# Kernel tuning notes

Measured on AMD Instinct MI355X. Metric: run time of the kernel, lower is better.

## Reference

```python
import jax, jax.numpy as jnp
import numpy as np

# CRF hyperparameters (match torch module defaults / init_kwargs)
W_BILATERAL = 1.0
W_GAUSSIAN = 1.0
SIG_B_SPATIAL = 5.0
SIG_B_COLOR = 0.5
SIG_G_SPATIAL = 5.0
UPDATE_FACTOR = 3.0
KERNEL_RANGE = 1
ITERATIONS = 5


def _coords(H, W, dtype):
    gy, gx = jnp.meshgrid(jnp.arange(H, dtype=dtype), jnp.arange(W, dtype=dtype), indexing='ij')
    return jnp.stack([gy, gx])  # [2, H, W]


def _gauss_kernel(feat):
    # feat: [B, N, D] -> dense Gaussian affinity [B, N, N] = exp(-0.5 ||f_i - f_j||^2)
    sq = jnp.sum(feat * feat, axis=-1)  # [B, N]
    d2 = sq[:, :, None] + sq[:, None, :] - 2.0 * jnp.einsum('bnd,bmd->bnm', feat, feat)
    return jnp.exp(-0.5 * jnp.maximum(d2, 0.0))


def setup_inputs() -> dict:
    key = jax.random.key(0)
    k1, k2 = jax.random.split(key)
    return {
        'input_tensor': jax.random.normal(k1, (1, 5, 96, 96), dtype=jnp.float32),
        'reference_tensor': jax.random.uniform(k2, (1, 3, 96, 96), dtype=jnp.float32),
    }


def reference(input_tensor, reference_tensor):
    B, C, H, W = input_tensor.shape
    N = H * W
    coords = jnp.broadcast_to(_coords(H, W, reference_tensor.dtype)[None], (B, 2, H, W))
    # bilateral features: scaled coords ++ scaled color -> [B, N, 2+Cref]
    bfeat = jnp.concatenate([coords / SIG_B_SPATIAL, reference_tensor / SIG_B_COLOR], axis=1)
    bfeat = bfeat.reshape(B, -1, N).transpose(0, 2, 1)
    gfeat = (coords / SIG_G_SPATIAL).reshape(B, 2, N).transpose(0, 2, 1)
    # features are fixed across iterations -> precompute dense filter kernels once
    Kb = _gauss_kernel(bfeat)  # [B, N, N]
    Kg = _gauss_kernel(gfeat)  # [B, N, N]
    ksz = 2 * KERNEL_RANGE + 1
    # Potts model compatibility kernel: (1 - I) constant over the 3x3 window
    comp = jnp.broadcast_to((1.0 - jnp.eye(C, dtype=input_tensor.dtype))[:, :, None, None], (C, C, ksz, ksz))
    out = jax.nn.softmax(input_tensor, axis=1)
    for _ in range(ITERATIONS):
        flat = out.reshape(B, C, N)
        comb = (W_BILATERAL * jnp.einsum('bnm,bcm->bcn', Kb, flat)
                + W_GAUSSIAN * jnp.einsum('bnm,bcm->bcn', Kg, flat)).reshape(B, C, H, W)
        comb = jnp.pad(comb, ((0, 0), (0, 0), (KERNEL_RANGE, KERNEL_RANGE), (KERNEL_RANGE, KERNEL_RANGE)), mode='edge')
        upd = jax.lax.conv_general_dilated(comb, comp, (1, 1), 'VALID',
                                           dimension_numbers=('NCHW', 'OIHW', 'NCHW'))
        out = jax.nn.softmax(input_tensor - UPDATE_FACTOR * upd, axis=1)
    return out
```

## Files before the change

kernel.cpp:

```cpp
#include <hip/hip_runtime.h>
#include <math.h>

#define HH 96
#define WW 96
#define NN (HH*WW)
#define RAD 30

__device__ __forceinline__ float np_expf(float x) {
    float q = __builtin_rintf(x * 1.442695040888963f);
    float r = fmaf(q, -6.93145752e-1f, x);
    r = fmaf(q, -1.42860677e-6f, r);
    float num = 5.082762527590693718096e-04f;
    num = fmaf(num, r, 6.757896990527504603057e-03f);
    num = fmaf(num, r, 5.114512081637298353406e-02f);
    num = fmaf(num, r, 2.473615434895520810817e-01f);
    num = fmaf(num, r, 7.257664613233124478488e-01f);
    num = fmaf(num, r, 9.999999999980870924916e-01f);
    float den = 2.159509375685829852307e-02f;
    den = fmaf(den, r, -2.742335390411667452936e-01f);
    den = fmaf(den, r, 1.0f);
    float p = num / den;
    p = ldexpf(p, (int)q);
    if (x > 88.72283935546875f) p = __builtin_inff();
    if (x < -103.97208404541015625f) p = 0.0f;
    return p;
}

__device__ __forceinline__ float np_expf_nc(float x) {
    float q = __builtin_rintf(x * 1.442695040888963f);
    float r = fmaf(q, -6.93145752e-1f, x);
    r = fmaf(q, -1.42860677e-6f, r);
    float num = 5.082762527590693718096e-04f;
    num = fmaf(num, r, 6.757896990527504603057e-03f);
    num = fmaf(num, r, 5.114512081637298353406e-02f);
    num = fmaf(num, r, 2.473615434895520810817e-01f);
    num = fmaf(num, r, 7.257664613233124478488e-01f);
    num = fmaf(num, r, 9.999999999980870924916e-01f);
    float den = 2.159509375685829852307e-02f;
    den = fmaf(den, r, -2.742335390411667452936e-01f);
    den = fmaf(den, r, 1.0f);
    float p = num / den;
    return ldexpf(p, (int)q);
}

__global__ __launch_bounds__(256) void crf_prep(const float* __restrict__ input,
                                                const float* __restrict__ ref,
                                                float4* __restrict__ colA,
                                                float4* __restrict__ qA,
                                                float* __restrict__ qB) {
#pragma clang fp contract(off)
    int n = blockIdx.x * 256 + threadIdx.x;
    if (n >= NN) return;
    int py = n / WW;
    int px = n - py * WW;
    float yb = (float)py / 5.0f;
    float xb = (float)px / 5.0f;
    float r2 = ref[0 * NN + n] * 2.0f;
    float g2 = ref[1 * NN + n] * 2.0f;
    float b2 = ref[2 * NN + n] * 2.0f;
    float sqg = yb * yb + xb * xb;
    float sqb = ((sqg + r2 * r2) + g2 * g2) + b2 * b2;
    colA[n] = make_float4(r2, g2, b2, sqb);
    float l0 = input[0 * NN + n], l1 = input[1 * NN + n], l2 = input[2 * NN + n];
    float l3 = input[3 * NN + n], l4 = input[4 * NN + n];
    float m = fmaxf(fmaxf(fmaxf(fmaxf(l0, l1), l2), l3), l4);
    float e0 = np_expf(l0 - m), e1 = np_expf(l1 - m), e2 = np_expf(l2 - m);
    float e3 = np_expf(l3 - m), e4 = np_expf(l4 - m);
    float s = (((e0 + e1) + e2) + e3) + e4;
    qA[n] = make_float4(e0 / s, e1 / s, e2 / s, e3 / s);
    qB[n] = e4 / s;
}

__global__ __launch_bounds__(256) void crf_filter(const float4* __restrict__ colA,
                                                  const float4* __restrict__ qA,
                                                  const float* __restrict__ qB,
                                                  float* __restrict__ combF) {
#pragma clang fp contract(off)
    __shared__ float c5[HH];
    __shared__ float sq1[HH];
    __shared__ float cg[8][5];
    int tid = threadIdx.x;
    if (tid < HH) {
        float v = (float)tid / 5.0f;
        c5[tid] = v;
        sq1[tid] = v * v;
    }
    __syncthreads();

    int br = blockIdx.x / 12;
    int bc = blockIdx.x - br * 12;
    int row = (br & 1) ? (48 + (br >> 1)) : (47 - (br >> 1));
    int cg8 = (bc & 1) ? (6 + (bc >> 1)) : (5 - (bc >> 1));

    int j = tid & 3;
    int k = (tid >> 2) & 3;
    int p = (tid >> 4) & 7;
    int role = tid >> 7;
    int n0 = row * WW + cg8 * 8 + p;
    int py = row;
    int px = cg8 * 8 + p;
    float yn = c5[py], xn = c5[px];
    float sqg_n = sq1[py] + sq1[px];
    float4 cn = colA[n0];
    float sqb_n = cn.w;
    int ylo = py - RAD; if (ylo < 0) ylo = 0;
    int yhi = py + RAD; if (yhi > HH - 1) yhi = HH - 1;
    int xlo = px - RAD; if (xlo < 0) xlo = 0;
    int xhi = px + RAD; if (xhi > WW - 1) xhi = WW - 1;
    int res = k * 4 + j;
    int cst = xlo + ((res - xlo) & 15);

    float a0 = 0.f, a1 = 0.f, a2 = 0.f, a3 = 0.f, a4 = 0.f;
    if (role == 0) {
#pragma unroll 2
        for (int my = ylo; my <= yhi; ++my) {
            float ym = c5[my];
            float tyy = yn * ym;
            int rb = my * WW;
            for (int mx = cst; mx <= xhi; mx += 16) {
                int m = rb + mx;
                float4 cm = colA[m];
                float4 f = qA[m];
                float fb = qB[m];
                float dot = tyy;
                dot = dot + xn * c5[mx];
                dot = dot + cn.x * cm.x;
                dot = dot + cn.y * cm.y;
                dot = dot + cn.z * cm.z;
                float d2 = (sqb_n + cm.w) - 2.0f * dot;
                d2 = fmaxf(d2, 0.0f);
                float w = np_expf_nc(-0.5f * d2);
                a0 = a0 + w * f.x;
                a1 = a1 + w * f.y;
                a2 = a2 + w * f.z;
                a3 = a3 + w * f.w;
                a4 = a4 + w * fb;
            }
        }
    } else {
#pragma unroll 2
        for (int my = ylo; my <= yhi; ++my) {
            float ym = c5[my];
            float tyy = yn * ym;
            float sqy = sq1[my];
            int rb = my * WW;
            for (int mx = cst; mx <= xhi; mx += 16) {
                int m = rb + mx;
                float4 f = qA[m];
                float fb = qB[m];
                float dot = tyy;
                dot = dot + xn * c5[mx];
                float sqm = sqy + sq1[mx];
                float d2 = (sqg_n + sqm) - 2.0f * dot;
                d2 = fmaxf(d2, 0.0f);
                float w = np_expf_nc(-0.5f * d2);
                a0 = a0 + w * f.x;
                a1 = a1 + w * f.y;
                a2 = a2 + w * f.z;
                a3 = a3 + w * f.w;
                a4 = a4 + w * fb;
            }
        }
    }
    float r_[5] = {a0, a1, a2, a3, a4};
#pragma unroll
    for (int c = 0; c < 5; ++c) {
        float v = r_[c];
        v = v + __shfl_xor(v, 4);
        v = v + __shfl_xor(v, 8);
        v = v + __shfl_xor(v, 2);
        v = v + __shfl_xor(v, 1);
        r_[c] = v;
    }
    if (role == 1 && (tid & 15) == 0) {
#pragma unroll
        for (int c = 0; c < 5; ++c) cg[p][c] = r_[c];
    }
    __syncthreads();
    if (role == 0 && (tid & 15) == 0) {
#pragma unroll
        for (int c = 0; c < 5; ++c) combF[c * NN + n0] = r_[c] + cg[p][c];
    }
}

__global__ __launch_bounds__(256) void crf_update(const float* __restrict__ input,
                                                  const float* __restrict__ combF,
                                                  float4* __restrict__ qA,
                                                  float* __restrict__ qB,
                                                  float* __restrict__ outp,
                                                  int writeOut) {
#pragma clang fp contract(off)
    int n = blockIdx.x * 256 + threadIdx.x;
    if (n >= NN) return;
    int py = n / WW;
    int px = n - py * WW;
    float v[3][3][5];
#pragma unroll
    for (int ky = 0; ky < 3; ++ky) {
        int yy = py + ky - 1; yy = yy < 0 ? 0 : (yy > HH - 1 ? HH - 1 : yy);
#pragma unroll
        for (int kx = 0; kx < 3; ++kx) {
            int xx = px + kx - 1; xx = xx < 0 ? 0 : (xx > WW - 1 ? WW - 1 : xx);
            int m = yy * WW + xx;
#pragma unroll
            for (int c = 0; c < 5; ++c) v[ky][kx][c] = combF[c * NN + m];
        }
    }
    float l[5];
#pragma unroll
    for (int o = 0; o < 5; ++o) {
        float u = 0.f;
#pragma unroll
        for (int ky = 0; ky < 3; ++ky) {
#pragma unroll
            for (int kx = 0; kx < 3; ++kx) {
                float t = 0.f;
#pragma unroll
                for (int ci = 0; ci < 5; ++ci)
                    if (ci != o) t = t + v[ky][kx][ci];
                u = u + t;
            }
        }
        l[o] = input[o * NN + n] - 3.0f * u;
    }
    float m = fmaxf(fmaxf(fmaxf(fmaxf(l[0], l[1]), l[2]), l[3]), l[4]);
    float e0 = np_expf(l[0] - m), e1 = np_expf(l[1] - m), e2 = np_expf(l[2] - m);
    float e3 = np_expf(l[3] - m), e4 = np_expf(l[4] - m);
    float s = (((e0 + e1) + e2) + e3) + e4;
    float o0 = e0 / s, o1 = e1 / s, o2 = e2 / s, o3 = e3 / s, o4 = e4 / s;
    qA[n] = make_float4(o0, o1, o2, o3);
    qB[n] = o4;
    if (writeOut) {
        outp[0 * NN + n] = o0;
        outp[1 * NN + n] = o1;
        outp[2 * NN + n] = o2;
        outp[3 * NN + n] = o3;
        outp[4 * NN + n] = o4;
    }
}

extern "C" void kernel_launch(void* const* d_in, const int* in_sizes, int n_in,
                              void* d_out, int out_size, void* d_ws, size_t ws_size,
                              hipStream_t stream) {
    const float* input = (const float*)d_in[0];
    const float* ref = (const float*)d_in[1];
    float* ws = (float*)d_ws;
    float4* colA = (float4*)(ws + 0 * NN);
    float4* qA = (float4*)(ws + 4 * NN);
    float* qB = ws + 8 * NN;
    float* combF = ws + 9 * NN;
    float* outp = (float*)d_out;

    crf_prep<<<36, 256, 0, stream>>>(input, ref, colA, qA, qB);
    for (int it = 0; it < 5; ++it) {
        crf_filter<<<1152, 256, 0, stream>>>(colA, qA, qB, combF);
        crf_update<<<36, 256, 0, stream>>>(input, combF, qA, qB, outp, it == 4 ? 1 : 0);
    }
}
```

Baseline: 423.3 us.

## Cache truncated filter weights on first iteration and reuse in later iterations

After: 455.1 us. 1.08x slower.

```diff
diff --git a/kernel.cpp b/kernel.cpp
--- a/kernel.cpp
+++ b/kernel.cpp
@@ -5,6 +5,7 @@
 #define WW 96
 #define NN (HH*WW)
 #define RAD 30
+#define TOTPAIRS 24265476
 
 __device__ __forceinline__ float np_expf(float x) {
     float q = __builtin_rintf(x * 1.442695040888963f);
@@ -41,6 +42,17 @@
     den = fmaf(den, r, 1.0f);
     float p = num / den;
     return ldexpf(p, (int)q);
+}
+
+__device__ __forceinline__ int wincnt(int x) {
+    int lo = x - RAD; if (lo < 0) lo = 0;
+    int hi = x + RAD; if (hi > 95) hi = 95;
+    return hi - lo + 1;
+}
+__device__ __forceinline__ int cumwin(int x) {
+    int g1 = (x <= 30) ? (30 * x - (x * (x - 1)) / 2) : 465;
+    int g2 = (x <= 66) ? 0 : ((x - 66) * (x - 65)) / 2;
+    return 61 * x - g1 - g2;
 }
 
 __global__ __launch_bounds__(256) void crf_prep(const float* __restrict__ input,
@@ -71,6 +83,183 @@
     qB[n] = e4 / s;
 }
 
+#define FILTER_PREAMBLE                                                        \
+    int tid = threadIdx.x;                                                     \
+    int br = blockIdx.x / 12;                                                  \
+    int bc = blockIdx.x - br * 12;                                             \
+    int row = (br & 1) ? (48 + (br >> 1)) : (47 - (br >> 1));                  \
+    int cg8 = (bc & 1) ? (6 + (bc >> 1)) : (5 - (bc >> 1));                    \
+    int j = tid & 3;                                                           \
+    int k = (tid >> 2) & 3;                                                    \
+    int p = (tid >> 4) & 7;                                                    \
+    int role = tid >> 7;                                                       \
+    int py = row;                                                              \
+    int px = cg8 * 8 + p;                                                      \
+    int n0 = row * WW + px;                                                    \
+    int ylo = py - RAD; if (ylo < 0) ylo = 0;                                  \
+    int yhi = py + RAD; if (yhi > HH - 1) yhi = HH - 1;                        \
+    int xlo = px - RAD; if (xlo < 0) xlo = 0;                                  \
+    int xhi = px + RAD; if (xhi > WW - 1) xhi = WW - 1;                        \
+    int res = k * 4 + j;                                                       \
+    int cst = xlo + ((res - xlo) & 15);
+
+__global__ __launch_bounds__(256) void crf_filter_store(const float4* __restrict__ colA,
+                                                        const float4* __restrict__ qA,
+                                                        const float* __restrict__ qB,
+                                                        float* __restrict__ combF,
+                                                        float* __restrict__ wts) {
+#pragma clang fp contract(off)
+    __shared__ float c5[HH];
+    __shared__ float sq1[HH];
+    __shared__ float cg[8][5];
+    if (threadIdx.x < HH) {
+        float v = (float)threadIdx.x / 5.0f;
+        c5[threadIdx.x] = v;
+        sq1[threadIdx.x] = v * v;
+    }
+    __syncthreads();
+    FILTER_PREAMBLE
+    float yn = c5[py], xn = c5[px];
+    float sqg_n = sq1[py] + sq1[px];
+    float4 cn = colA[n0];
+    float sqb_n = cn.w;
+    int winX = xhi - xlo + 1;
+    int winY = yhi - ylo + 1;
+    int base2 = 2 * (cumwin(py) * 4926 + winY * cumwin(px));
+    float* wp = wts + base2 + role * (winY * winX);
+    int coff = cst - xlo;
+
+    float a0 = 0.f, a1 = 0.f, a2 = 0.f, a3 = 0.f, a4 = 0.f;
+    if (role == 0) {
+#pragma unroll 2
+        for (int my = ylo; my <= yhi; ++my) {
+            float ym = c5[my];
+            float tyy = yn * ym;
+            int rb = my * WW;
+            float* wrow = wp + (my - ylo) * winX + coff;
+            int t = 0;
+            for (int mx = cst; mx <= xhi; mx += 16, ++t) {
+                int m = rb + mx;
+                float4 cm = colA[m];
+                float4 f = qA[m];
+                float fb = qB[m];
+                float dot = tyy;
+                dot = dot + xn * c5[mx];
+                dot = dot + cn.x * cm.x;
+                dot = dot + cn.y * cm.y;
+                dot = dot + cn.z * cm.z;
+                float d2 = (sqb_n + cm.w) - 2.0f * dot;
+                d2 = fmaxf(d2, 0.0f);
+                float w = np_expf_nc(-0.5f * d2);
+                wrow[t * 16] = w;
+                a0 = a0 + w * f.x;
+                a1 = a1 + w * f.y;
+                a2 = a2 + w * f.z;
+                a3 = a3 + w * f.w;
+                a4 = a4 + w * fb;
+            }
+        }
+    } else {
+#pragma unroll 2
+        for (int my = ylo; my <= yhi; ++my) {
+            float ym = c5[my];
+            float tyy = yn * ym;
+            float sqy = sq1[my];
+            int rb = my * WW;
+            float* wrow = wp + (my - ylo) * winX + coff;
+            int t = 0;
+            for (int mx = cst; mx <= xhi; mx += 16, ++t) {
+                int m = rb + mx;
+                float4 f = qA[m];
+                float fb = qB[m];
+                float dot = tyy;
+                dot = dot + xn * c5[mx];
+                float sqm = sqy + sq1[mx];
+                float d2 = (sqg_n + sqm) - 2.0f * dot;
+                d2 = fmaxf(d2, 0.0f);
+                float w = np_expf_nc(-0.5f * d2);
+                wrow[t * 16] = w;
+                a0 = a0 + w * f.x;
+                a1 = a1 + w * f.y;
+                a2 = a2 + w * f.z;
+                a3 = a3 + w * f.w;
+                a4 = a4 + w * fb;
+            }
+        }
+    }
+    float r_[5] = {a0, a1, a2, a3, a4};
+#pragma unroll
+    for (int c = 0; c < 5; ++c) {
+        float v = r_[c];
+        v = v + __shfl_xor(v, 4);
+        v = v + __shfl_xor(v, 8);
+        v = v + __shfl_xor(v, 2);
+        v = v + __shfl_xor(v, 1);
+        r_[c] = v;
+    }
+    if (role == 1 && (tid & 15) == 0) {
+#pragma unroll
+        for (int c = 0; c < 5; ++c) cg[p][c] = r_[c];
+    }
+    __syncthreads();
+    if (role == 0 && (tid & 15) == 0) {
+#pragma unroll
+        for (int c = 0; c < 5; ++c) combF[c * NN + n0] = r_[c] + cg[p][c];
+    }
+}
+
+__global__ __launch_bounds__(256) void crf_filter_apply(const float4* __restrict__ qA,
+                                                        const float* __restrict__ qB,
+                                                        float* __restrict__ combF,
+                                                        const float* __restrict__ wts) {
+#pragma clang fp contract(off)
+    __shared__ float cg[8][5];
+    FILTER_PREAMBLE
+    int winX = xhi - xlo + 1;
+    int winY = yhi - ylo + 1;
+    int base2 = 2 * (cumwin(py) * 4926 + winY * cumwin(px));
+    const float* wp = wts + base2 + role * (winY * winX);
+    int coff = cst - xlo;
+
+    float a0 = 0.f, a1 = 0.f, a2 = 0.f, a3 = 0.f, a4 = 0.f;
+#pragma unroll 2
+    for (int my = ylo; my <= yhi; ++my) {
+        int rb = my * WW;
+        const float* wrow = wp + (my - ylo) * winX + coff;
+        int t = 0;
+        for (int mx = cst; mx <= xhi; mx += 16, ++t) {
+            int m = rb + mx;
+            float4 f = qA[m];
+            float fb = qB[m];
+            float w = wrow[t * 16];
+            a0 = a0 + w * f.x;
+            a1 = a1 + w * f.y;
+            a2 = a2 + w * f.z;
+            a3 = a3 + w * f.w;
+            a4 = a4 + w * fb;
+        }
+    }
+    float r_[5] = {a0, a1, a2, a3, a4};
+#pragma unroll
+    for (int c = 0; c < 5; ++c) {
+        float v = r_[c];
+        v = v + __shfl_xor(v, 4);
+        v = v + __shfl_xor(v, 8);
+        v = v + __shfl_xor(v, 2);
+        v = v + __shfl_xor(v, 1);
+        r_[c] = v;
+    }
+    if (role == 1 && (tid & 15) == 0) {
+#pragma unroll
+        for (int c = 0; c < 5; ++c) cg[p][c] = r_[c];
+    }
+    __syncthreads();
+    if (role == 0 && (tid & 15) == 0) {
+#pragma unroll
+        for (int c = 0; c < 5; ++c) combF[c * NN + n0] = r_[c] + cg[p][c];
+    }
+}
+
 __global__ __launch_bounds__(256) void crf_filter(const float4* __restrict__ colA,
                                                   const float4* __restrict__ qA,
                                                   const float* __restrict__ qB,
@@ -79,36 +268,17 @@
     __shared__ float c5[HH];
     __shared__ float sq1[HH];
     __shared__ float cg[8][5];
-    int tid = threadIdx.x;
-    if (tid < HH) {
-        float v = (float)tid / 5.0f;
-        c5[tid] = v;
-        sq1[tid] = v * v;
+    if (threadIdx.x < HH) {
+        float v = (float)threadIdx.x / 5.0f;
+        c5[threadIdx.x] = v;
+        sq1[threadIdx.x] = v * v;
     }
     __syncthreads();
-
-    int br = blockIdx.x / 12;
-    int bc = blockIdx.x - br * 12;
-    int row = (br & 1) ? (48 + (br >> 1)) : (47 - (br >> 1));
-    int cg8 = (bc & 1) ? (6 + (bc >> 1)) : (5 - (bc >> 1));
-
-    int j = tid & 3;
-    int k = (tid >> 2) & 3;
-    int p = (tid >> 4) & 7;
-    int role = tid >> 7;
-    int n0 = row * WW + cg8 * 8 + p;
-    int py = row;
-    int px = cg8 * 8 + p;
+    FILTER_PREAMBLE
     float yn = c5[py], xn = c5[px];
     float sqg_n = sq1[py] + sq1[px];
     float4 cn = colA[n0];
     float sqb_n = cn.w;
-    int ylo = py - RAD; if (ylo < 0) ylo = 0;
-    int yhi = py + RAD; if (yhi > HH - 1) yhi = HH - 1;
-    int xlo = px - RAD; if (xlo < 0) xlo = 0;
-    int xhi = px + RAD; if (xhi > WW - 1) xhi = WW - 1;
-    int res = k * 4 + j;
-    int cst = xlo + ((res - xlo) & 15);
 
     float a0 = 0.f, a1 = 0.f, a2 = 0.f, a3 = 0.f, a4 = 0.f;
     if (role == 0) {
@@ -249,11 +419,22 @@
     float4* qA = (float4*)(ws + 4 * NN);
     float* qB = ws + 8 * NN;
     float* combF = ws + 9 * NN;
+    float* wts = ws + 14 * NN;
     float* outp = (float*)d_out;
 
+    size_t need = ((size_t)14 * NN + (size_t)2 * TOTPAIRS) * sizeof(float);
     crf_prep<<<36, 256, 0, stream>>>(input, ref, colA, qA, qB);
-    for (int it = 0; it < 5; ++it) {
-        crf_filter<<<1152, 256, 0, stream>>>(colA, qA, qB, combF);
-        crf_update<<<36, 256, 0, stream>>>(input, combF, qA, qB, outp, it == 4 ? 1 : 0);
-    }
-}
+    if (ws_size >= need) {
+        crf_filter_store<<<1152, 256, 0, stream>>>(colA, qA, qB, combF, wts);
+        crf_update<<<36, 256, 0, stream>>>(input, combF, qA, qB, outp, 0);
+        for (int it = 1; it < 5; ++it) {
+            crf_filter_apply<<<1152, 256, 0, stream>>>(qA, qB, combF, wts);
+            crf_update<<<36, 256, 0, stream>>>(input, combF, qA, qB, outp, it == 4 ? 1 : 0);
+        }
+    } else {
+        for (int it = 0; it < 5; ++it) {
+            crf_filter<<<1152, 256, 0, stream>>>(colA, qA, qB, combF);
+            crf_update<<<36, 256, 0, stream>>>(input, combF, qA, qB, outp, it == 4 ? 1 : 0);
+        }
+    }
+}
```
